# Performance work log

Hardware: AMD Instinct MI355X
Metric: run time of the kernel (lower is better)

Reference implementation:

```python
import jax, jax.numpy as jnp
import numpy as np


def setup_inputs() -> dict:
    key = jax.random.key(0)
    n, b, E, H, P = 2048, 2, 1024, 16, 16
    ks = jax.random.split(key, 8)
    wscale = 1.0 / np.sqrt(E)  # xavier-ish
    return {
        "query": jax.random.normal(ks[0], (n, b, E), jnp.float32),
        "pquery": jax.random.normal(ks[1], (P, b, E), jnp.float32),
        "Wpq": jax.random.normal(ks[2], (E, E), jnp.float32) * wscale,
        "bpq": jnp.zeros((E,), jnp.float32),
        "Wk": jax.random.normal(ks[3], (E, E), jnp.float32) * wscale,
        "bk": jnp.zeros((E,), jnp.float32),
        "Wv": jax.random.normal(ks[4], (E, E), jnp.float32) * wscale,
        "bv": jnp.zeros((E,), jnp.float32),
        "Wo": jax.random.normal(ks[5], (E, E), jnp.float32) * wscale,
        "bo": jnp.zeros((E,), jnp.float32),
        "num_heads": 16,
    }


def reference(query, pquery, Wpq, bpq, Wk, bk, Wv, bv, Wo, bo, num_heads):
    # query: (n, b, E), pquery: (P, b, E)  [Time x Batch x Channel]
    n, b, E = query.shape
    P = pquery.shape[0]
    H = num_heads
    hd = E // H
    scaling = hd ** -0.5

    # pq projection -> (b, H, P, hd), scaled
    pq = (pquery @ Wpq.T + bpq).reshape(P, b, H, hd).transpose(1, 2, 0, 3) * scaling
    qh = query.reshape(n, b, H, hd)
    # pattn_weights: (b*H, n, P) -- compressed attention logits
    pattn = jnp.einsum('nbhd,bhpd->bhnp', qh, pq).reshape(b * H, n, P)

    def to_bh(x):  # (n,b,E) -> (b*H, n, hd)
        return x.reshape(n, b, H, hd).transpose(1, 2, 0, 3).reshape(b * H, n, hd)

    q = to_bh(query * scaling)
    k = to_bh(query @ Wk.T + bk)
    v = to_bh(query @ Wv.T + bv)

    # Causal prefix softmax over pattn columns. softmax over prefix j<i per
    # column p is exp(pattn[j,p]) / S_i[p] with S_i[p] = sum_{j<i} exp(pattn[j,p]).
    # Shift by per-column global max for stability (softmax shift-invariant).
    m = jnp.max(pattn, axis=1, keepdims=True)
    Eexp = jnp.exp(pattn - m)                       # (BH, n, P)
    S = jnp.cumsum(Eexp, axis=1) - Eexp             # exclusive cumsum (BH, n, P)
    Ssafe = jnp.where(S > 0, S, 1.0)                # row 0 -> zeros numerators anyway

    # Stage 1: attn_weights[i] = q_i @ sum_{j<i} k_j^T softmax(pattn)_j
    KE = k[:, :, :, None] * Eexp[:, :, None, :]     # (BH, n, hd, P)
    Ncum = jnp.cumsum(KE, axis=1) - KE              # exclusive
    attn_weights = jnp.einsum('bnd,bndp->bnp', q, Ncum) / Ssafe  # (BH, n, P)

    aw = jax.nn.softmax(attn_weights, axis=-1)      # (BH, n, P); dropout=0.0

    # Stage 2: attn[i] = aw_i @ sum_{j<i} softmax(pattn)_j v_j^T
    EV = Eexp[:, :, :, None] * v[:, :, None, :]     # (BH, n, P, hd)
    Mcum = jnp.cumsum(EV, axis=1) - EV              # exclusive
    out = jnp.einsum('bnp,bnpd->bnd', aw / Ssafe, Mcum)  # (BH, n, hd)

    attn = out.reshape(b, H, n, hd).transpose(2, 0, 1, 3).reshape(n, b, E)
    attn = attn @ Wo.T + bo

    # need_weights=True, need_head_weights=False -> mean over heads
    aw_avg = aw.reshape(b, H, n, P).mean(axis=1)    # (b, n, P)
    return attn, aw_avg
```

## Files before the change

### kernel.cpp

```cpp
#include <hip/hip_runtime.h>
#include <cstddef>

#define N_TOK 2048
#define BATCH 2
#define EMB   1024
#define NH    16
#define HD    64
#define NP    16
#define BHN   32
#define CHK   64
#define NCHK  32
#define SCALING 0.125f

typedef __attribute__((ext_vector_type(8))) short short8;
typedef __attribute__((ext_vector_type(4))) float f32x4;

typedef __attribute__((address_space(1))) const void gvoid;
typedef __attribute__((address_space(3))) void lvoid;
__device__ __forceinline__ void gload16(const void* g, void* l) {
  __builtin_amdgcn_global_load_lds((gvoid*)g, (lvoid*)l, 16, 0, 0);
}

__device__ __forceinline__ unsigned short f2bf(float f) {
  unsigned u = __float_as_uint(f);
  u += 0x7FFFu + ((u >> 16) & 1u);
  return (unsigned short)(u >> 16);
}
__device__ __forceinline__ float bf2f(unsigned short b) {
  return __uint_as_float((unsigned)b << 16);
}

__global__ __launch_bounds__(256) void prep_pq_kernel(
    const float* __restrict__ query, const float* __restrict__ Wk,
    const float* __restrict__ Wv, const float* __restrict__ Wo,
    const float* __restrict__ bk, const float* __restrict__ bv,
    const float* __restrict__ pquery, const float* __restrict__ Wpq,
    const float* __restrict__ bpq,
    unsigned short* __restrict__ qbf, unsigned short* __restrict__ wkvbf,
    unsigned short* __restrict__ wobf, float* __restrict__ bkv,
    unsigned short* __restrict__ pq_sb)
{
  const int b = blockIdx.x, t = threadIdx.x;
  if (b < 512) {
    __shared__ float xs[EMB];
    __shared__ float part[4][64];
    const int r = b >> 4, seg = b & 15;
    const int p = r >> 1, ib = r & 1;
    const int el = t & 63, ks = t >> 6;
    const int e = seg * 64 + el;
    for (int l = t; l < EMB; l += 256) xs[l] = pquery[(size_t)r * EMB + l];
    __syncthreads();
    const float* wrow = &Wpq[(size_t)e * EMB + ks * 256];
    const float* xp = &xs[ks * 256];
    float acc = 0.f;
    #pragma unroll 8
    for (int cc = 0; cc < 256; cc += 4) {
      const float4 w4 = *(const float4*)&wrow[cc];
      acc += xp[cc] * w4.x + xp[cc + 1] * w4.y + xp[cc + 2] * w4.z + xp[cc + 3] * w4.w;
    }
    part[ks][el] = acc;
    __syncthreads();
    if (ks == 0) {
      float s = part[0][el] + part[1][el] + part[2][el] + part[3][el];
      s = (s + bpq[e]) * SCALING;
      const int h = e >> 6, d = e & 63;
      pq_sb[((size_t)(ib * NH + h) * NP + p) * HD + d] = f2bf(s);
    }
  } else {
    const int tid = (b - 512) * 256 + t;
    const int NT = 1024 * 256;
    for (int i = tid; i < 1835008; i += NT) {
      const float* src; unsigned short* dst; int off;
      if (i < 1048576)      { src = query; dst = qbf;             off = i; }
      else if (i < 1310720) { src = Wk;    dst = wkvbf;           off = i - 1048576; }
      else if (i < 1572864) { src = Wv;    dst = wkvbf + 1048576; off = i - 1310720; }
      else                  { src = Wo;    dst = wobf;            off = i - 1572864; }
      const float4 v = *(const float4*)&src[(size_t)off * 4];
      ushort4 o;
      o.x = f2bf(v.x); o.y = f2bf(v.y); o.z = f2bf(v.z); o.w = f2bf(v.w);
      *(ushort4*)&dst[(size_t)off * 4] = o;
    }
    if (tid < 512) {
      const int j = tid * 4;
      if (j < 1024) *(float4*)&bkv[j] = *(const float4*)&bk[j];
      else          *(float4*)&bkv[j] = *(const float4*)&bv[j - 1024];
    }
  }
}

__global__ __launch_bounds__(256) void kv_gemm_kernel(
    const unsigned short* __restrict__ Xb, const unsigned short* __restrict__ Wb,
    const float* __restrict__ bias, unsigned short* __restrict__ Y0,
    unsigned short* __restrict__ Y1)
{
  __shared__ unsigned short As[2][4096];
  __shared__ unsigned short Bs[2][4096];
  const int t = threadIdx.x;
  const int L = blockIdx.x;
  const int b = (L & 7) * 64 + (L >> 3);
  const int m0 = (b >> 4) * 128, n0 = (b & 15) * 128;
  const int lane = t & 63, w = t >> 6, wr = w >> 1, wc = w & 1;
  const int lr = lane & 15, lg = lane >> 4;
  const int srow = t >> 2, scol = (t & 3) << 3;
  const unsigned short* xa = &Xb[(size_t)(m0 + srow) * 1024 + scol];
  const unsigned short* xc = xa + (size_t)64 * 1024;
  const unsigned short* wp = &Wb[(size_t)(n0 + srow) * 1024 + scol];
  const unsigned short* wq = wp + (size_t)64 * 1024;
  f32x4 acc[4][4] = {};

  gload16(xa, &As[0][t * 8]);
  gload16(xc, &As[0][2048 + t * 8]);
  gload16(wp, &Bs[0][t * 8]);
  gload16(wq, &Bs[0][2048 + t * 8]);
  __syncthreads();
  int cur = 0;
  for (int ks = 0; ks < 32; ++ks) {
    if (ks < 31) {
      const int k1 = (ks + 1) * 32;
      gload16(xa + k1, &As[cur ^ 1][t * 8]);
      gload16(xc + k1, &As[cur ^ 1][2048 + t * 8]);
      gload16(wp + k1, &Bs[cur ^ 1][t * 8]);
      gload16(wq + k1, &Bs[cur ^ 1][2048 + t * 8]);
    }
    short8 av[4], bv[4];
    #pragma unroll
    for (int m = 0; m < 4; ++m) av[m] = *(const short8*)&As[cur][(wr * 64 + m * 16 + lr) * 32 + lg * 8];
    #pragma unroll
    for (int n = 0; n < 4; ++n) bv[n] = *(const short8*)&Bs[cur][(wc * 64 + n * 16 + lr) * 32 + lg * 8];
    #pragma unroll
    for (int m = 0; m < 4; ++m)
      #pragma unroll
      for (int n = 0; n < 4; ++n)
        acc[m][n] = __builtin_amdgcn_mfma_f32_16x16x32_bf16(av[m], bv[n], acc[m][n], 0, 0, 0);
    __syncthreads();
    cur ^= 1;
  }

  unsigned short* reg = (wr == 0) ? &As[0][0] : &Bs[0][0];
  #pragma unroll
  for (int n = 0; n < 4; ++n) {
    const int cl = wc * 64 + n * 16 + lr;
    const float bcol = bias[n0 + cl];
    #pragma unroll
    for (int m = 0; m < 4; ++m) {
      const int rl = (m * 16 + lg * 4);
      #pragma unroll
      for (int q = 0; q < 4; ++q)
        reg[(rl + q) * 128 + cl] = f2bf(acc[m][n][q] + bcol);
    }
  }
  __syncthreads();
  unsigned short* dd = (n0 < 1024) ? Y0 : Y1;
  const int n0l = n0 & 1023;
  const int chunk = t & 15;
  #pragma unroll
  for (int pass = 0; pass < 8; ++pass) {
    const int row = pass * 16 + (t >> 4);
    const unsigned short* rg = (row < 64) ? &As[0][0] : &Bs[0][0];
    const uint4 v = *(const uint4*)&rg[(row & 63) * 128 + chunk * 8];
    *(uint4*)&dd[(size_t)(m0 + row) * 1024 + n0l + chunk * 8] = v;
  }
}

__global__ __launch_bounds__(256) void pattn_totals_kernel(
    const unsigned short* __restrict__ qbf, const unsigned short* __restrict__ pq_sb,
    const unsigned short* __restrict__ Kbf, const unsigned short* __restrict__ Vbf,
    unsigned short* __restrict__ peb, unsigned short* __restrict__ Tkb,
    unsigned short* __restrict__ Tvb, float* __restrict__ Tsc)
{
  const int c = blockIdx.x, bh = blockIdx.y;
  const int ib = bh >> 4, h = bh & 15;
  const int t = threadIdx.x;
  const int i0 = c * CHK;
  const int lane = t & 63, w = t >> 6;
  const int lr = lane & 15, lg = lane >> 4;
  const int wrow = w * 16;

  __shared__ unsigned short KT[64][80];
  __shared__ unsigned short VT[64][80];
  __shared__ unsigned short EbT[16][80];
  __shared__ float Ef[64][20];
  __shared__ float tspart[4][16];

  #pragma unroll
  for (int it = 0; it < 2; ++it) {
    const int task = t + it * 256;
    const int j = task & 63, dg = task >> 6;
    const size_t g = ((size_t)(i0 + j) * BATCH + ib) * EMB + h * HD + dg * 8;
    const uint4 ku = *(const uint4*)&Kbf[g];
    const uint4 vu = *(const uint4*)&Vbf[g];
    const unsigned short* kk = (const unsigned short*)&ku;
    const unsigned short* vv = (const unsigned short*)&vu;
    #pragma unroll
    for (int e = 0; e < 8; ++e) { KT[dg * 8 + e][j] = kk[e]; VT[dg * 8 + e][j] = vv[e]; }
  }

  {
    const size_t qg = ((size_t)(i0 + wrow + lr) * BATCH + ib) * EMB + h * HD;
    short8 avq0 = *(const short8*)&qbf[qg + lg * 8];
    short8 avq1 = *(const short8*)&qbf[qg + 32 + lg * 8];
    const size_t pb = (size_t)bh * 1024 + (size_t)lr * 64;
    short8 bp0 = *(const short8*)&pq_sb[pb + lg * 8];
    short8 bp1 = *(const short8*)&pq_sb[pb + 32 + lg * 8];
    f32x4 lacc = {};
    lacc = __builtin_amdgcn_mfma_f32_16x16x32_bf16(avq0, bp0, lacc, 0, 0, 0);
    lacc = __builtin_amdgcn_mfma_f32_16x16x32_bf16(avq1, bp1, lacc, 0, 0, 0);
    #pragma unroll
    for (int q = 0; q < 4; ++q) {
      const int i = wrow + lg * 4 + q;
      const float e = expf(lacc[q]);
      const unsigned short eb = f2bf(e);
      peb[(size_t)bh * (N_TOK * NP) + (size_t)(i0 + i) * NP + lr] = eb;
      Ef[i][lr] = e;
      EbT[lr][i] = eb;
    }
  }
  __syncthreads();

  if (t < 64) {
    const int p = t & 15, qq = t >> 4;
    float s = 0.f;
    #pragma unroll
    for (int jj = 0; jj < 16; ++jj) s += Ef[qq * 16 + jj][p];
    tspart[qq][p] = s;
  }

  short8 ae0 = *(const short8*)&EbT[lr][lg * 8];
  short8 ae1 = *(const short8*)&EbT[lr][32 + lg * 8];
  const size_t tb = (size_t)(bh * NCHK + c) * 1024;

  {
    f32x4 ka = {};
    short8 bk0 = *(const short8*)&KT[w * 16 + lr][lg * 8];
    short8 bk1 = *(const short8*)&KT[w * 16 + lr][32 + lg * 8];
    ka = __builtin_amdgcn_mfma_f32_16x16x32_bf16(ae0, bk0, ka, 0, 0, 0);
    ka = __builtin_amdgcn_mfma_f32_16x16x32_bf16(ae1, bk1, ka, 0, 0, 0);
    #pragma unroll
    for (int q = 0; q < 4; ++q) Tkb[tb + (lg * 4 + q) * 64 + w * 16 + lr] = f2bf(ka[q]);
  }
  {
    f32x4 va = {};
    short8 av0 = *(const short8*)&VT[w * 16 + lr][lg * 8];
    short8 av1 = *(const short8*)&VT[w * 16 + lr][32 + lg * 8];
    va = __builtin_amdgcn_mfma_f32_16x16x32_bf16(av0, ae0, va, 0, 0, 0);
    va = __builtin_amdgcn_mfma_f32_16x16x32_bf16(av1, ae1, va, 0, 0, 0);
    #pragma unroll
    for (int q = 0; q < 4; ++q) Tvb[tb + (w * 16 + lg * 4 + q) * 16 + lr] = f2bf(va[q]);
  }
  __syncthreads();
  if (t < 16)
    Tsc[(size_t)(bh * NCHK + c) * 16 + t] =
        tspart[0][t] + tspart[1][t] + tspart[2][t] + tspart[3][t];
}

__global__ __launch_bounds__(256) void chunk_scan_kernel(
    unsigned short* __restrict__ Tkb, unsigned short* __restrict__ Tvb,
    float* __restrict__ Ts)
{
  const int bh = blockIdx.x, y = blockIdx.y, t = threadIdx.x;
  const int slot = y * 256 + t;
  unsigned short* arr = (slot < 1024) ? Tkb : Tvb;
  const int e = slot & 1023;
  const size_t base = (size_t)bh * (NCHK * 1024) + e;
  float v[NCHK];
  #pragma unroll
  for (int c = 0; c < NCHK; ++c) v[c] = bf2f(arr[base + (size_t)c * 1024]);
  float run = 0.f;
  #pragma unroll
  for (int c = 0; c < NCHK; ++c) { arr[base + (size_t)c * 1024] = f2bf(run); run += v[c]; }
  if (y == 7 && t < 16) {
    const size_t sb = (size_t)bh * (NCHK * 16) + t;
    float s[NCHK];
    #pragma unroll
    for (int c = 0; c < NCHK; ++c) s[c] = Ts[sb + c * 16];
    float rs = 0.f;
    #pragma unroll
    for (int c = 0; c < NCHK; ++c) { Ts[sb + c * 16] = rs; rs += s[c]; }
  }
}

__global__ __launch_bounds__(256) void attn_mfma_kernel(
    const unsigned short* __restrict__ qbf, const unsigned short* __restrict__ Kbf,
    const unsigned short* __restrict__ Vbf, const unsigned short* __restrict__ peb,
    const unsigned short* __restrict__ Tkb, const unsigned short* __restrict__ Tvb,
    const float* __restrict__ Ts, unsigned short* __restrict__ aw_bufb,
    unsigned short* __restrict__ outpre)
{
  const int c = blockIdx.x, bh = blockIdx.y;
  const int ib = bh >> 4, h = bh & 15;
  const int t = threadIdx.x;
  const int i0 = c * CHK;
  const int lane = t & 63, w = t >> 6;
  const int ws = w * 16;
  const int lr = lane & 15, lg = lane >> 4;
  const int nsl = (w >> 1) + 1;
  const short8 zero8 = {0, 0, 0, 0, 0, 0, 0, 0};

  __shared__ unsigned short VT[64][80];
  __shared__ unsigned short Ab[64][80];
  __shared__ unsigned short EbT[16][80];
  __shared__ unsigned short Gb[64][40];

  const size_t qg = ((size_t)(i0 + ws + lr) * BATCH + ib) * EMB + h * HD;
  short8 avq0 = *(const short8*)&qbf[qg + lg * 8];
  short8 avq1 = *(const short8*)&qbf[qg + 32 + lg * 8];

  #pragma unroll
  for (int it = 0; it < 2; ++it) {
    const int task = t + it * 256;
    const int j = task & 63, dg = task >> 6;
    const size_t g = ((size_t)(i0 + j) * BATCH + ib) * EMB + h * HD + dg * 8;
    const uint4 vu = *(const uint4*)&Vbf[g];
    const unsigned short* vv = (const unsigned short*)&vu;
    #pragma unroll
    for (int e = 0; e < 8; ++e) VT[dg * 8 + e][j] = vv[e];
  }
  {
    const int j = t >> 2, p0 = (t & 3) << 2;
    const ushort4 e4 = *(const ushort4*)&peb[(size_t)bh * (N_TOK * NP) + (size_t)(i0 + j) * NP + p0];
    EbT[p0][j] = e4.x; EbT[p0 + 1][j] = e4.y; EbT[p0 + 2][j] = e4.z; EbT[p0 + 3][j] = e4.w;
  }
  __syncthreads();

  f32x4 sacc[4] = {};
  #pragma unroll
  for (int n = 0; n < 4; ++n) {
    const size_t kg = ((size_t)(i0 + n * 16 + lr) * BATCH + ib) * EMB + h * HD;
    short8 bk0 = *(const short8*)&Kbf[kg + lg * 8];
    short8 bk1 = *(const short8*)&Kbf[kg + 32 + lg * 8];
    if (n <= w) {
      sacc[n] = __builtin_amdgcn_mfma_f32_16x16x32_bf16(avq0, bk0, sacc[n], 0, 0, 0);
      sacc[n] = __builtin_amdgcn_mfma_f32_16x16x32_bf16(avq1, bk1, sacc[n], 0, 0, 0);
    }
  }
  #pragma unroll
  for (int q = 0; q < 4; ++q)
    if (lr >= lg * 4 + q) sacc[w][q] = 0.f;
  for (int n = 0; n < 2 * nsl; ++n)
    #pragma unroll
    for (int q = 0; q < 4; ++q)
      Ab[ws + lg * 4 + q][n * 16 + lr] = f2bf(sacc[n][q]);

  short8 bve0 = *(const short8*)&EbT[lr][lg * 8];
  short8 bve1 = *(const short8*)&EbT[lr][32 + lg * 8];

  f32x4 wacc = {};
  {
    const size_t nb = (size_t)(bh * NCHK + c) * 1024 + (size_t)lr * 64 + lg * 8;
    short8 bn0 = *(const short8*)&Tkb[nb];
    short8 bn1 = *(const short8*)&Tkb[nb + 32];
    wacc = __builtin_amdgcn_mfma_f32_16x16x32_bf16(avq0, bn0, wacc, 0, 0, 0);
    wacc = __builtin_amdgcn_mfma_f32_16x16x32_bf16(avq1, bn1, wacc, 0, 0, 0);
  }
  for (int ks = 0; ks < nsl; ++ks) {
    short8 aa = *(const short8*)&Ab[ws + lr][ks * 32 + lg * 8];
    wacc = __builtin_amdgcn_mfma_f32_16x16x32_bf16(aa, ks ? bve1 : bve0, wacc, 0, 0, 0);
  }
  const float s0 = Ts[(size_t)(bh * NCHK + c) * 16 + lr];
  f32x4 scacc = {s0, s0, s0, s0};
  for (int ks = 0; ks < nsl; ++ks) {
    const int jb = ks * 32 + lg * 8;
    const int irow = ws + lr;
    short8 ones;
    #pragma unroll
    for (int e = 0; e < 8; ++e) ones[e] = (short)((jb + e < irow) ? 0x3F80 : 0);
    scacc = __builtin_amdgcn_mfma_f32_16x16x32_bf16(ones, ks ? bve1 : bve0, scacc, 0, 0, 0);
  }

  const size_t awbase = (size_t)bh * (N_TOK * NP) + (size_t)i0 * NP;
  #pragma unroll
  for (int q = 0; q < 4; ++q) {
    const int il = lg * 4 + q;
    const float ssum = scacc[q];
    const float ssafe = (ssum > 0.f) ? ssum : 1.f;
    const float wv = SCALING * wacc[q] / ssafe;
    float m = wv;
    #pragma unroll
    for (int off = 1; off < 16; off <<= 1) m = fmaxf(m, __shfl_xor(m, off, 64));
    const float e = expf(wv - m);
    float ss = e;
    #pragma unroll
    for (int off = 1; off < 16; off <<= 1) ss += __shfl_xor(ss, off, 64);
    const float aw = e / ss;
    aw_bufb[awbase + (size_t)(ws + il) * NP + lr] = f2bf(aw);
    const float g = aw / ssafe;
    Gb[ws + il][lr] = f2bf(g);
    Gb[ws + il][lr + 16] = 0;
  }

  short8 ga = *(const short8*)&Gb[ws + lr][lg * 8];
  f32x4 bacc[4] = {};
  #pragma unroll
  for (int n = 0; n < 4; ++n) {
    const size_t eg = (size_t)bh * (N_TOK * NP) + (size_t)(i0 + n * 16 + lr) * NP + (lg & 1) * 8;
    short8 bl = *(const short8*)&peb[eg];
    short8 be = (lg < 2) ? bl : zero8;
    if (n <= w)
      bacc[n] = __builtin_amdgcn_mfma_f32_16x16x32_bf16(ga, be, bacc[n], 0, 0, 0);
  }
  #pragma unroll
  for (int q = 0; q < 4; ++q)
    if (lr >= lg * 4 + q) bacc[w][q] = 0.f;
  for (int n = 0; n < 2 * nsl; ++n)
    #pragma unroll
    for (int q = 0; q < 4; ++q)
      Ab[ws + lg * 4 + q][n * 16 + lr] = f2bf(bacc[n][q]);

  f32x4 oacc[4] = {};
  #pragma unroll
  for (int dn = 0; dn < 4; ++dn) {
    const size_t mb = (size_t)(bh * NCHK + c) * 1024 + (size_t)(dn * 16 + lr) * 16 + (lg & 1) * 8;
    short8 bmv = *(const short8*)&Tvb[mb];
    short8 bm = (lg < 2) ? bmv : zero8;
    oacc[dn] = __builtin_amdgcn_mfma_f32_16x16x32_bf16(ga, bm, oacc[dn], 0, 0, 0);
  }
  for (int ks = 0; ks < nsl; ++ks) {
    short8 ab = *(const short8*)&Ab[ws + lr][ks * 32 + lg * 8];
    #pragma unroll
    for (int dn = 0; dn < 4; ++dn) {
      short8 bv = *(const short8*)&VT[dn * 16 + lr][ks * 32 + lg * 8];
      oacc[dn] = __builtin_amdgcn_mfma_f32_16x16x32_bf16(ab, bv, oacc[dn], 0, 0, 0);
    }
  }

  __syncthreads();
  unsigned short* ot = &VT[0][0];
  #pragma unroll
  for (int dn = 0; dn < 4; ++dn)
    #pragma unroll
    for (int q = 0; q < 4; ++q)
      ot[(ws + lg * 4 + q) * 64 + dn * 16 + lr] = f2bf(oacc[dn][q]);
  __syncthreads();
  {
    const int row = t >> 2, ch = (t & 3) * 2;
    const size_t gbase = ((size_t)(i0 + row) * BATCH + ib) * EMB + h * HD;
    *(uint4*)&outpre[gbase + ch * 8] = *(const uint4*)&ot[row * 64 + ch * 8];
    *(uint4*)&outpre[gbase + (ch + 1) * 8] = *(const uint4*)&ot[row * 64 + (ch + 1) * 8];
  }
}

__global__ __launch_bounds__(256) void o_aw_kernel(
    const unsigned short* __restrict__ Xb, const unsigned short* __restrict__ Wb,
    const float* __restrict__ bias, float* __restrict__ Yf,
    const unsigned short* __restrict__ aw_bufb, float* __restrict__ out_aw)
{
  __shared__ unsigned short As[2][4096];
  __shared__ unsigned short Bs[2][2048];
  const int L = blockIdx.x, t = threadIdx.x;
  if (L < 512) {
    const int b = (L & 7) * 64 + (L >> 3);
    const int m0 = (b >> 4) * 128, n0 = (b & 15) * 64;
    const int lane = t & 63, w = t >> 6, wr = w >> 1, wc = w & 1;
    const int lr = lane & 15, lg = lane >> 4;
    const int srow = t >> 2, scol = (t & 3) << 3;
    const unsigned short* xa = &Xb[(size_t)(m0 + srow) * 1024 + scol];
    const unsigned short* xc = &Xb[(size_t)(m0 + srow + 64) * 1024 + scol];
    const unsigned short* wp = &Wb[(size_t)(n0 + srow) * 1024 + scol];
    f32x4 acc[4][2] = {};

    gload16(xa, &As[0][t * 8]);
    gload16(xc, &As[0][2048 + t * 8]);
    gload16(wp, &Bs[0][t * 8]);
    __syncthreads();
    int cur = 0;
    for (int ks = 0; ks < 32; ++ks) {
      if (ks < 31) {
        const int k1 = (ks + 1) * 32;
        gload16(xa + k1, &As[cur ^ 1][t * 8]);
        gload16(xc + k1, &As[cur ^ 1][2048 + t * 8]);
        gload16(wp + k1, &Bs[cur ^ 1][t * 8]);
      }
      short8 av[4], bv[2];
      #pragma unroll
      for (int m = 0; m < 4; ++m) av[m] = *(const short8*)&As[cur][(wr * 64 + m * 16 + lr) * 32 + lg * 8];
      #pragma unroll
      for (int n = 0; n < 2; ++n) bv[n] = *(const short8*)&Bs[cur][(wc * 32 + n * 16 + lr) * 32 + lg * 8];
      #pragma unroll
      for (int m = 0; m < 4; ++m)
        #pragma unroll
        for (int n = 0; n < 2; ++n)
          acc[m][n] = __builtin_amdgcn_mfma_f32_16x16x32_bf16(av[m], bv[n], acc[m][n], 0, 0, 0);
      __syncthreads();
      cur ^= 1;
    }
    #pragma unroll
    for (int n = 0; n < 2; ++n) {
      const int gcol = n0 + wc * 32 + n * 16 + lr;
      const float bcol = bias[gcol];
      #pragma unroll
      for (int m = 0; m < 4; ++m) {
        const int row0 = m0 + wr * 64 + m * 16 + lg * 4;
        #pragma unroll
        for (int q = 0; q < 4; ++q)
          Yf[(size_t)(row0 + q) * 1024 + gcol] = acc[m][n][q] + bcol;
      }
    }
  } else {
    const int idx = (L - 512) * 256 + t;
    const int p = idx & 15;
    const int i = (idx >> 4) & 2047;
    const int ib = idx >> 15;
    float s = 0.f;
    for (int hh = 0; hh < NH; ++hh)
      s += bf2f(aw_bufb[((size_t)(ib * NH + hh) * N_TOK + i) * NP + p]);
    out_aw[idx] = s * (1.f / 16.f);
  }
}

extern "C" void kernel_launch(void* const* d_in, const int* in_sizes, int n_in,
                              void* d_out, int out_size, void* d_ws, size_t ws_size,
                              hipStream_t stream) {
  const float* query  = (const float*)d_in[0];
  const float* pquery = (const float*)d_in[1];
  const float* Wpq    = (const float*)d_in[2];
  const float* bpq    = (const float*)d_in[3];
  const float* Wk     = (const float*)d_in[4];
  const float* bk     = (const float*)d_in[5];
  const float* Wv     = (const float*)d_in[6];
  const float* bv     = (const float*)d_in[7];
  const float* Wo     = (const float*)d_in[8];
  const float* bo     = (const float*)d_in[9];
  float* out = (float*)d_out;
  float* ws  = (float*)d_ws;

  float* Ts     = ws;
  float* bkv    = Ts + 16384;
  unsigned short* Tkb   = (unsigned short*)(bkv + 2048);
  unsigned short* Tvb   = Tkb + 1048576;
  unsigned short* pq_sb = Tvb + 1048576;
  unsigned short* peb   = pq_sb + 32768;
  unsigned short* awb   = peb + 1048576;
  unsigned short* qbf   = awb + 1048576;
  unsigned short* Kbf   = qbf + 4194304;
  unsigned short* Vbf   = Kbf + 4194304;
  unsigned short* wkvbf = Vbf + 4194304;
  unsigned short* wobf  = wkvbf + 2097152;
  unsigned short* opbf  = wobf + 1048576;

  prep_pq_kernel<<<1536, 256, 0, stream>>>(query, Wk, Wv, Wo, bk, bv, pquery, Wpq, bpq,
                                           qbf, wkvbf, wobf, bkv, pq_sb);
  kv_gemm_kernel<<<512, 256, 0, stream>>>(qbf, wkvbf, bkv, Kbf, Vbf);
  pattn_totals_kernel<<<dim3(NCHK, BHN), 256, 0, stream>>>(qbf, pq_sb, Kbf, Vbf,
                                                           peb, Tkb, Tvb, Ts);
  chunk_scan_kernel<<<dim3(BHN, 8), 256, 0, stream>>>(Tkb, Tvb, Ts);
  attn_mfma_kernel<<<dim3(NCHK, BHN), 256, 0, stream>>>(qbf, Kbf, Vbf, peb, Tkb, Tvb, Ts,
                                                        awb, opbf);
  o_aw_kernel<<<768, 256, 0, stream>>>(opbf, wobf, bo, out, awb, out + 4194304);
}
```

Before: 108.2 us.

## Fuse chunk-prefix scan into pattn_totals via last-block atomic counter

Removes the separate chunk_scan kernel launch. Each pattn_totals block increments a per-(batch,head) atomic counter after writing its chunk totals. The last block to finish for that head then runs the exclusive scan over all chunks in place. This saves a launch and its grid-wide dependency, but the scan now runs on only 32 blocks, one per head, each doing 8x more serial work than before. The counters are reset in the prep kernel.

```diff
diff --git a/kernel.cpp b/kernel.cpp
--- a/kernel.cpp
+++ b/kernel.cpp
@@ -38,7 +38,7 @@
     const float* __restrict__ bpq,
     unsigned short* __restrict__ qbf, unsigned short* __restrict__ wkvbf,
     unsigned short* __restrict__ wobf, float* __restrict__ bkv,
-    unsigned short* __restrict__ pq_sb)
+    unsigned short* __restrict__ pq_sb, unsigned* __restrict__ cnt)
 {
   const int b = blockIdx.x, t = threadIdx.x;
   if (b < 512) {
@@ -67,6 +67,7 @@
       pq_sb[((size_t)(ib * NH + h) * NP + p) * HD + d] = f2bf(s);
     }
   } else {
+    if (b == 512 && t < BHN) cnt[t] = 0;
     const int tid = (b - 512) * 256 + t;
     const int NT = 1024 * 256;
     for (int i = tid; i < 1835008; i += NT) {
@@ -166,7 +167,8 @@
     const unsigned short* __restrict__ qbf, const unsigned short* __restrict__ pq_sb,
     const unsigned short* __restrict__ Kbf, const unsigned short* __restrict__ Vbf,
     unsigned short* __restrict__ peb, unsigned short* __restrict__ Tkb,
-    unsigned short* __restrict__ Tvb, float* __restrict__ Tsc)
+    unsigned short* __restrict__ Tvb, float* __restrict__ Tsc,
+    unsigned* __restrict__ cnt)
 {
   const int c = blockIdx.x, bh = blockIdx.y;
   const int ib = bh >> 4, h = bh & 15;
@@ -181,6 +183,7 @@
   __shared__ unsigned short EbT[16][80];
   __shared__ float Ef[64][20];
   __shared__ float tspart[4][16];
+  __shared__ unsigned lastflag;
 
   #pragma unroll
   for (int it = 0; it < 2; ++it) {
@@ -251,31 +254,39 @@
   if (t < 16)
     Tsc[(size_t)(bh * NCHK + c) * 16 + t] =
         tspart[0][t] + tspart[1][t] + tspart[2][t] + tspart[3][t];
-}
-
-__global__ __launch_bounds__(256) void chunk_scan_kernel(
-    unsigned short* __restrict__ Tkb, unsigned short* __restrict__ Tvb,
-    float* __restrict__ Ts)
-{
-  const int bh = blockIdx.x, y = blockIdx.y, t = threadIdx.x;
-  const int slot = y * 256 + t;
-  unsigned short* arr = (slot < 1024) ? Tkb : Tvb;
-  const int e = slot & 1023;
-  const size_t base = (size_t)bh * (NCHK * 1024) + e;
-  float v[NCHK];
-  #pragma unroll
-  for (int c = 0; c < NCHK; ++c) v[c] = bf2f(arr[base + (size_t)c * 1024]);
-  float run = 0.f;
-  #pragma unroll
-  for (int c = 0; c < NCHK; ++c) { arr[base + (size_t)c * 1024] = f2bf(run); run += v[c]; }
-  if (y == 7 && t < 16) {
-    const size_t sb = (size_t)bh * (NCHK * 16) + t;
-    float s[NCHK];
-    #pragma unroll
-    for (int c = 0; c < NCHK; ++c) s[c] = Ts[sb + c * 16];
-    float rs = 0.f;
-    #pragma unroll
-    for (int c = 0; c < NCHK; ++c) { Ts[sb + c * 16] = rs; rs += s[c]; }
+
+  __syncthreads();
+  if (t == 0) {
+    __threadfence();
+    lastflag = atomicAdd(&cnt[bh], 1u);
+  }
+  __syncthreads();
+  if (lastflag == NCHK - 1) {
+    __threadfence();
+    #pragma unroll
+    for (int s = 0; s < 8; ++s) {
+      const int slot = t + s * 256;
+      unsigned short* arr = (slot < 1024) ? Tkb : Tvb;
+      const int e = slot & 1023;
+      const size_t base = (size_t)bh * (NCHK * 1024) + e;
+      float run = 0.f;
+      #pragma unroll
+      for (int c2 = 0; c2 < NCHK; ++c2) {
+        const float v = bf2f(arr[base + (size_t)c2 * 1024]);
+        arr[base + (size_t)c2 * 1024] = f2bf(run);
+        run += v;
+      }
+    }
+    if (t < 16) {
+      const size_t sb = (size_t)bh * (NCHK * 16) + t;
+      float rs = 0.f;
+      #pragma unroll
+      for (int c2 = 0; c2 < NCHK; ++c2) {
+        const float sv = Tsc[sb + c2 * 16];
+        Tsc[sb + c2 * 16] = rs;
+        rs += sv;
+      }
+    }
   }
 }
 
@@ -525,7 +536,8 @@
 
   float* Ts     = ws;
   float* bkv    = Ts + 16384;
-  unsigned short* Tkb   = (unsigned short*)(bkv + 2048);
+  unsigned* cnt = (unsigned*)(bkv + 2048);
+  unsigned short* Tkb   = (unsigned short*)(bkv + 2048 + 512);
   unsigned short* Tvb   = Tkb + 1048576;
   unsigned short* pq_sb = Tvb + 1048576;
   unsigned short* peb   = pq_sb + 32768;
@@ -538,11 +550,10 @@
   unsigned short* opbf  = wobf + 1048576;
 
   prep_pq_kernel<<<1536, 256, 0, stream>>>(query, Wk, Wv, Wo, bk, bv, pquery, Wpq, bpq,
-                                           qbf, wkvbf, wobf, bkv, pq_sb);
+                                           qbf, wkvbf, wobf, bkv, pq_sb, cnt);
   kv_gemm_kernel<<<512, 256, 0, stream>>>(qbf, wkvbf, bkv, Kbf, Vbf);
   pattn_totals_kernel<<<dim3(NCHK, BHN), 256, 0, stream>>>(qbf, pq_sb, Kbf, Vbf,
-                                                           peb, Tkb, Tvb, Ts);
-  chunk_scan_kernel<<<dim3(BHN, 8), 256, 0, stream>>>(Tkb, Tvb, Ts);
+                                                           peb, Tkb, Tvb, Ts, cnt);
   attn_mfma_kernel<<<dim3(NCHK, BHN), 256, 0, stream>>>(qbf, Kbf, Vbf, peb, Tkb, Tvb, Ts,
                                                         awb, opbf);
   o_aw_kernel<<<768, 256, 0, stream>>>(opbf, wobf, bo, out, awb, out + 4194304);
```

Result: slower. 167.6 us (+54.9%).
